# Optimization experiments

Measured on AMD Instinct MI355X. Metric: run time of the kernel, lower is better.

Reference implementation:

```python
import jax, jax.numpy as jnp
from jax import lax
import numpy as np

DIM = 800
FEAT = 192
LAYERS = 5
BLOCK_SZ = [32, 192, 192, 192, 192]
BLOCK_RNG = [0, 32, 224, 416, 608, 800]
HALF = 27  # image_size//4//2 - 1 with image_size=224
EPS = 1e-5


def conv2d(x, w, stride=1, pad=0, groups=1):
    return lax.conv_general_dilated(
        x, w, (stride, stride), [(pad, pad), (pad, pad)],
        dimension_numbers=("NCHW", "OIHW", "NCHW"),
        feature_group_count=groups)


def _bcast(v):
    return v[None, :, None, None]


def setup_inputs() -> dict:
    key = jax.random.key(0)
    ks = jax.random.split(key, 22)
    B = 32
    s = 0.05
    return {
        "x": jax.random.normal(ks[0], (B, 3, 224, 224), jnp.float32),
        "ds_w1": jax.random.normal(ks[1], (16, 3, 3, 3), jnp.float32) * s,
        "ds_b1": jax.random.normal(ks[2], (16,), jnp.float32) * s,
        "bn1_g": jax.random.uniform(ks[3], (16,), jnp.float32) + 0.5,
        "bn1_b": jax.random.normal(ks[4], (16,), jnp.float32) * s,
        "bn1_m": jax.random.normal(ks[5], (16,), jnp.float32) * s,
        "bn1_v": jax.random.uniform(ks[6], (16,), jnp.float32) + 0.5,
        "ds_dw": jax.random.normal(ks[7], (16, 1, 3, 3), jnp.float32) * s,
        "ds_dwb": jax.random.normal(ks[8], (16,), jnp.float32) * s,
        "ds_w2": jax.random.normal(ks[9], (32, 16, 1, 1), jnp.float32) * s,
        "ds_b2": jax.random.normal(ks[10], (32,), jnp.float32) * s,
        "bn2_g": jax.random.uniform(ks[11], (32,), jnp.float32) + 0.5,
        "bn2_b": jax.random.normal(ks[12], (32,), jnp.float32) * s,
        "bn2_m": jax.random.normal(ks[13], (32,), jnp.float32) * s,
        "bn2_v": jax.random.uniform(ks[14], (32,), jnp.float32) + 0.5,
        "conv_dw": jax.random.normal(ks[15], (DIM, 1, 3, 3), jnp.float32) * s,
        "gw": jax.random.normal(ks[16], (DIM, DIM), jnp.float32) * s,
        "in_gamma": jax.random.uniform(ks[17], (DIM,), jnp.float32) + 0.5,
        "in_beta": jax.random.normal(ks[18], (DIM,), jnp.float32) * s,
        "fc_w": jax.random.normal(ks[19], (1000, FEAT), jnp.float32) * s,
        "fc_b": jax.random.normal(ks[20], (1000,), jnp.float32) * s,
    }


def _forward(x, ds_w1, ds_b1, bn1_g, bn1_b, bn1_m, bn1_v, ds_dw, ds_dwb,
             ds_w2, ds_b2, bn2_g, bn2_b, bn2_m, bn2_v, conv_dw, gw,
             in_gamma, in_beta, fc_w, fc_b):
    # ---- downsample stem: conv3x3 s2 -> BN -> ReLU -> dwconv3x3 s2 -> conv1x1 -> BN
    h = conv2d(x, ds_w1, 2, 1) + _bcast(ds_b1)
    h = (h - _bcast(bn1_m)) * _bcast(bn1_g * lax.rsqrt(bn1_v + EPS)) + _bcast(bn1_b)
    h = jax.nn.relu(h)
    h = conv2d(h, ds_dw, 2, 1, groups=16) + _bcast(ds_dwb)
    h = conv2d(h, ds_w2, 1, 0) + _bcast(ds_b2)
    h = (h - _bcast(bn2_m)) * _bcast(bn2_g * lax.rsqrt(bn2_v + EPS)) + _bcast(bn2_b)
    B, _, H, W = h.shape  # (B, 32, 56, 56)
    h = jnp.concatenate([h, jnp.zeros((B, DIM - 32, H, W), h.dtype)], axis=1)

    # ---- per-block InstanceNorm -> ReLU -> depthwise conv -> sliced 1x1 graph conv -> residual
    for i in range(LAYERS):
        s, r0, r1 = BLOCK_SZ[i], BLOCK_RNG[i], BLOCK_RNG[i + 1]
        xa = h[:, :s]
        mu = xa.mean((2, 3), keepdims=True)
        var = ((xa - mu) ** 2).mean((2, 3), keepdims=True)
        xa = (xa - mu) * lax.rsqrt(var + EPS)
        xa = xa * _bcast(in_gamma[r0:r1]) + _bcast(in_beta[r0:r1])
        xa = jax.nn.relu(xa)
        xa = conv2d(xa, conv_dw[r0:r1], 1, 1, groups=s)
        row0 = min(r1, DIM - FEAT)
        xa = jnp.einsum("oc,bchw->bohw", gw[row0:, r0:r1], xa)
        h = (h[:, s:] if i < LAYERS - 1 else h[:, -FEAT:]) + xa

    # ---- AvgPool2d(2) over the 3x3 crop keeps only the top-left 2x2 mean
    out = h[:, :, HALF - 1:HALF + 1, HALF - 1:HALF + 1].mean((2, 3))
    return out @ fc_w.T + fc_b


def reference(x, ds_w1, ds_b1, bn1_g, bn1_b, bn1_m, bn1_v, ds_dw, ds_dwb,
              ds_w2, ds_b2, bn2_g, bn2_b, bn2_m, bn2_v, conv_dw, gw,
              in_gamma, in_beta, fc_w, fc_b):
    return _forward(x, ds_w1, ds_b1, bn1_g, bn1_b, bn1_m, bn1_v, ds_dw, ds_dwb,
                    ds_w2, ds_b2, bn2_g, bn2_b, bn2_m, bn2_v, conv_dw, gw,
                    in_gamma, in_beta, fc_w, fc_b)
```

## Files before the change

### kernel.cpp

```cpp
#include <hip/hip_runtime.h>
#include <stddef.h>

#define EPS 1e-5f
#define N_HW 3136
#define G 32
#define NG (G * N_HW)
#define DIMC 800
#define NTILE 49

typedef unsigned short u16;
typedef __attribute__((ext_vector_type(8))) short short8;
typedef __attribute__((ext_vector_type(4))) float floatx4;

__device__ __forceinline__ u16 f2b(float f) {
  unsigned u = __float_as_uint(f);
  u += 0x7FFFu + ((u >> 16) & 1u);
  return (u16)(u >> 16);
}
__device__ __forceinline__ float blo(unsigned u) { return __uint_as_float(u << 16); }
__device__ __forceinline__ float bhi(unsigned u) { return __uint_as_float(u & 0xFFFF0000u); }

static const size_t XA_OFF  = 0;
static const size_t H0_OFF  = 122028032ull;
static const size_t BLK_OFF = 134873088ull;
static const size_t GWB_OFF = 173408256ull;
static const size_t STS_OFF = 174688256ull;
static const size_t STQ_OFF = 174712832ull;
static const size_t PAT_OFF = 174737408ull;
static const size_t M4_OFF  = 179456000ull;
static const size_t MH_OFF  = M4_OFF + 6144 * 4;
static const size_t OP_OFF  = MH_OFF + 6144 * 4;
static const size_t NEED    = OP_OFF + 6144 * 4;

__global__ __launch_bounds__(256) void gw2bf(const float* __restrict__ gw, u16* __restrict__ gwb) {
  int i = (blockIdx.x * 256 + threadIdx.x) * 4;
  float4 v = *(const float4*)(gw + i);
  gwb[i + 0] = f2b(v.x); gwb[i + 1] = f2b(v.y);
  gwb[i + 2] = f2b(v.z); gwb[i + 3] = f2b(v.w);
}

__global__ __launch_bounds__(256) void zero_stats(float* __restrict__ p) {
  p[blockIdx.x * 256 + threadIdx.x] = 0.f;
}

#define XT_PITCH 226
#define XT_CH (17 * XT_PITCH)
__global__ __launch_bounds__(256) void stem_conv1(
    const float* __restrict__ xg, const float* __restrict__ w, const float* __restrict__ b1,
    const float* __restrict__ g, const float* __restrict__ bb,
    const float* __restrict__ m, const float* __restrict__ v,
    float* __restrict__ h1) {
  __shared__ float xt[3 * XT_CH];
  __shared__ float wt[16 * 27];
  __shared__ float mulc[16], addc[16];
  int blk = blockIdx.x;
  int s = blk % 14;
  int bg = blk / 14;
  int tid = threadIdx.x;

  for (int e = tid; e < 432; e += 256) wt[e] = w[e];
  if (tid < 16) {
    float A = g[tid] * rsqrtf(v[tid] + EPS);
    mulc[tid] = A;
    addc[tid] = (b1[tid] - m[tid]) * A + bb[tid];
  }
  int iy0 = 16 * s - 1;
  for (int e = tid; e < 3 * XT_CH; e += 256) {
    int ci = e / XT_CH;
    int rem = e - ci * XT_CH;
    int r = rem / XT_PITCH;
    int cc = rem - r * XT_PITCH;
    int iy = iy0 + r, ix = cc - 1;
    float val = 0.f;
    if (iy >= 0 && iy < 224 && ix >= 0 && ix < 224)
      val = xg[((size_t)(bg * 3 + ci)) * 224 * 224 + iy * 224 + ix];
    xt[e] = val;
  }
  __syncthreads();

  for (int p = tid; p < 8 * 112; p += 256) {
    int oyl = p / 112, ox = p - oyl * 112;
    float xv[27];
#pragma unroll
    for (int ci = 0; ci < 3; ci++)
#pragma unroll
      for (int ky = 0; ky < 3; ky++)
#pragma unroll
        for (int kx = 0; kx < 3; kx++)
          xv[ci * 9 + ky * 3 + kx] = xt[ci * XT_CH + (2 * oyl + ky) * XT_PITCH + 2 * ox + kx];
    int oy = 8 * s + oyl;
#pragma unroll
    for (int c = 0; c < 16; c++) {
      float acc = 0.f;
#pragma unroll
      for (int t = 0; t < 27; t++) acc += xv[t] * wt[c * 27 + t];
      float y = acc * mulc[c] + addc[c];
      h1[(size_t)(c * G + bg) * 12544 + oy * 112 + ox] = fmaxf(y, 0.f);
    }
  }
}

__global__ __launch_bounds__(256) void stem_dw(
    const float* __restrict__ h1, const float* __restrict__ dw, const float* __restrict__ dwb,
    float* __restrict__ h2) {
  int idx = blockIdx.x * 256 + threadIdx.x;
  int q = idx % N_HW;
  int t = idx / N_HW;
  int bg = t & (G - 1);
  int c = t >> 5;
  int qy = q / 56, qx = q % 56;
  const float* plane = h1 + (size_t)(c * G + bg) * 12544;
  float acc = dwb[c];
#pragma unroll
  for (int ky = 0; ky < 3; ky++) {
    int iy = qy * 2 - 1 + ky;
    if (iy < 0 || iy >= 112) continue;
#pragma unroll
    for (int kx = 0; kx < 3; kx++) {
      int ix = qx * 2 - 1 + kx;
      if (ix < 0 || ix >= 112) continue;
      acc += plane[iy * 112 + ix] * dw[c * 9 + ky * 3 + kx];
    }
  }
  h2[idx] = acc;
}

__global__ __launch_bounds__(256) void stem_pw(
    const float* __restrict__ h2, const float* __restrict__ w2, const float* __restrict__ b2,
    const float* __restrict__ g, const float* __restrict__ bb,
    const float* __restrict__ m, const float* __restrict__ v,
    float* __restrict__ H0) {
  int idx = blockIdx.x * 256 + threadIdx.x;
  int q = idx % N_HW;
  int t = idx / N_HW;
  int bg = t & (G - 1);
  int o = t >> 5;
  float acc = b2[o];
#pragma unroll
  for (int c = 0; c < 16; c++) acc += w2[o * 16 + c] * h2[(size_t)(c * G + bg) * N_HW + q];
  float y = (acc - m[o]) * (g[o] * rsqrtf(v[o] + EPS)) + bb[o];
  H0[idx] = y;
}

template <typename T>
__global__ __launch_bounds__(256) void dw_fused(
    const T* __restrict__ base, const float* __restrict__ cdw,
    const float* __restrict__ in_g, const float* __restrict__ in_b,
    u16* __restrict__ XA, int cdwoff) {
  __shared__ float sm[58 * 58];
  __shared__ float wred[8];
  int blk = blockIdx.x;
  int cl = blk >> 5;
  int c = cdwoff + cl;
  int tid = threadIdx.x;

  if (tid < 58) { sm[tid] = 0.f; sm[57 * 58 + tid] = 0.f; }
  if (tid >= 64 && tid < 120) { int r = tid - 63; sm[r * 58] = 0.f; sm[r * 58 + 57] = 0.f; }

  const T* row = base + (size_t)blk * N_HW;
  float s = 0.f, s2 = 0.f;
  for (int i = tid; i < 392; i += 256) {
    float vals[8];
    if constexpr (sizeof(T) == 2) {
      uint4 u = *(const uint4*)((const u16*)row + i * 8);
      vals[0] = blo(u.x); vals[1] = bhi(u.x);
      vals[2] = blo(u.y); vals[3] = bhi(u.y);
      vals[4] = blo(u.z); vals[5] = bhi(u.z);
      vals[6] = blo(u.w); vals[7] = bhi(u.w);
    } else {
      float4 v0 = *(const float4*)((const float*)row + i * 8);
      float4 v1 = *(const float4*)((const float*)row + i * 8 + 4);
      vals[0] = v0.x; vals[1] = v0.y; vals[2] = v0.z; vals[3] = v0.w;
      vals[4] = v1.x; vals[5] = v1.y; vals[6] = v1.z; vals[7] = v1.w;
    }
    int p = i * 8;
    int y = p / 56, x = p - y * 56;
    float* d = &sm[(y + 1) * 58 + x + 1];
#pragma unroll
    for (int e = 0; e < 8; e++) {
      d[e] = vals[e];
      s += vals[e];
      s2 += vals[e] * vals[e];
    }
  }
#pragma unroll
  for (int o = 32; o > 0; o >>= 1) {
    s += __shfl_down(s, o);
    s2 += __shfl_down(s2, o);
  }
  if ((tid & 63) == 0) { wred[(tid >> 6) * 2] = s; wred[(tid >> 6) * 2 + 1] = s2; }
  __syncthreads();
  float ts = (wred[0] + wred[2]) + (wred[4] + wred[6]);
  float tq = (wred[1] + wred[3]) + (wred[5] + wred[7]);
  float mean = ts * (1.f / N_HW);
  float var = fmaxf(tq * (1.f / N_HW) - mean * mean, 0.f);
  float sc = in_g[c] * rsqrtf(var + EPS);
  float sh = in_b[c] - mean * sc;

  for (int i = tid; i < N_HW; i += 256) {
    int y = i / 56, x = i - y * 56;
    int pos = (y + 1) * 58 + x + 1;
    sm[pos] = fmaxf(sm[pos] * sc + sh, 0.f);
  }
  __syncthreads();

  float w0 = cdw[c * 9 + 0], w1 = cdw[c * 9 + 1], w2 = cdw[c * 9 + 2];
  float w3 = cdw[c * 9 + 3], w4 = cdw[c * 9 + 4], w5 = cdw[c * 9 + 5];
  float w6 = cdw[c * 9 + 6], w7 = cdw[c * 9 + 7], w8 = cdw[c * 9 + 8];
  u16* outp = XA + (size_t)blk * N_HW;
  for (int pp = tid; pp < N_HW / 2; pp += 256) {
    int p = pp * 2;
    int y = p / 56, x = p - y * 56;
    const float* p0 = &sm[y * 58 + x];
    float a0 = p0[0] * w0 + p0[1] * w1 + p0[2] * w2
             + p0[58] * w3 + p0[59] * w4 + p0[60] * w5
             + p0[116] * w6 + p0[117] * w7 + p0[118] * w8;
    float a1 = p0[1] * w0 + p0[2] * w1 + p0[3] * w2
             + p0[59] * w3 + p0[60] * w4 + p0[61] * w5
             + p0[117] * w6 + p0[118] * w7 + p0[119] * w8;
    unsigned pk = (unsigned)f2b(a0) | ((unsigned)f2b(a1) << 16);
    *(unsigned*)&outp[p] = pk;
  }
}

template <int MODE>
__global__ __launch_bounds__(256) void gemm_mfma(
    const u16* __restrict__ A, const u16* __restrict__ B, u16* __restrict__ C,
    float* __restrict__ statS, float* __restrict__ statQ, float* __restrict__ patchf,
    int K) {
  __shared__ u16 As[2][96][40];
  __shared__ u16 Bs[2][32][64];
  int nwg = gridDim.x;
  int cpx = nwg >> 3;
  int j = (blockIdx.x & 7) * cpx + (blockIdx.x >> 3);
  int jm = j & 1;
  int jc = j >> 1;
  int n0 = jc * 64;
  int m0 = jm * 96;
  int tid = threadIdx.x;
  int wave = tid >> 6, lane = tid & 63;
  int wm = wave >> 1, wn = wave & 1;
  int lg = lane >> 4, li = lane & 15;
  floatx4 acc[3][2] = {};

  int ar = tid >> 2, ak = (tid & 3) * 8;
  int bk = tid >> 3, bn = (tid & 7) * 8;
  int bnx = bn ^ ((bk >> 3) << 4);
  const u16* Ag = A + (size_t)(m0 + ar) * DIMC + ak;
  const u16* Bg = B + (size_t)bk * NG + n0 + bn;

  int nt = K / 32;
  uint4 ra0 = *(const uint4*)(Ag);
  uint4 ra1 = {0, 0, 0, 0};
  if (ar < 32) ra1 = *(const uint4*)(Ag + (size_t)64 * DIMC);
  uint4 rb_w = *(const uint4*)(Bg);
  uint4 rb_f = (nt > 1) ? *(const uint4*)(Bg + (size_t)32 * NG) : rb_w;

  for (int t = 0; t < nt; t++) {
    int cur = t & 1;
    *(uint4*)&As[cur][ar][ak] = ra0;
    if (ar < 32) *(uint4*)&As[cur][ar + 64][ak] = ra1;
    *(uint4*)&Bs[cur][bk][bnx] = rb_w;
    uint4 rb_new;
    bool pfA = (t + 1 < nt);
    bool pfB = (t + 2 < nt);
    if (pfA) {
      const u16* ag = Ag + (size_t)(t + 1) * 32;
      ra0 = *(const uint4*)(ag);
      if (ar < 32) ra1 = *(const uint4*)(ag + (size_t)64 * DIMC);
    }
    if (pfB)
      rb_new = *(const uint4*)(Bg + (size_t)(t + 2) * 32 * NG);
    __syncthreads();
    short8 aF[3];
#pragma unroll
    for (int mi = 0; mi < 3; mi++)
      aF[mi] = *(const short8*)&As[cur][wm * 48 + mi * 16 + li][lg * 8];
#pragma unroll
    for (int ni = 0; ni < 2; ni++) {
      int colx = ((wn * 32 + ni * 16) ^ (lg << 4)) + li;
      short8 bF;
#pragma unroll
      for (int e = 0; e < 8; e++) bF[e] = (short)Bs[cur][lg * 8 + e][colx];
#pragma unroll
      for (int mi = 0; mi < 3; mi++)
        acc[mi][ni] = __builtin_amdgcn_mfma_f32_16x16x32_bf16(aF[mi], bF, acc[mi][ni], 0, 0, 0);
    }
    __syncthreads();
    rb_w = rb_f;
    if (pfB) rb_f = rb_new;
  }

  if constexpr (MODE == 0) {
#pragma unroll
    for (int mi = 0; mi < 3; mi++) {
#pragma unroll
      for (int ni = 0; ni < 2; ni++) {
        int row = m0 + wm * 48 + mi * 16 + lg * 4;
        int col = n0 + wn * 32 + ni * 16 + li;
        u16* cp = C + (size_t)row * NG + col;
#pragma unroll
        for (int r = 0; r < 4; r++) cp[(size_t)r * NG] = f2b(acc[mi][ni][r]);
      }
    }
  } else {
    int bg = jc / NTILE;
    int tile = jc % NTILE;
#pragma unroll
    for (int mi = 0; mi < 3; mi++) {
#pragma unroll
      for (int r = 0; r < 4; r++) {
        float v0 = acc[mi][0][r], v1 = acc[mi][1][r];
        float s = v0 + v1;
        float q = v0 * v0 + v1 * v1;
#pragma unroll
        for (int msk = 1; msk < 16; msk <<= 1) {
          s += __shfl_xor(s, msk);
          q += __shfl_xor(q, msk);
        }
        if (li == 0) {
          int row = m0 + wm * 48 + mi * 16 + lg * 4 + r;
          atomicAdd(&statS[row * 32 + bg], s);
          atomicAdd(&statQ[row * 32 + bg], q);
        }
      }
    }
    if (tile >= 22 && tile <= 24) {
#pragma unroll
      for (int mi = 0; mi < 3; mi++) {
#pragma unroll
        for (int ni = 0; ni < 2; ni++) {
          int row = m0 + wm * 48 + mi * 16 + lg * 4;
          int pc = (tile - 22) * 64 + wn * 32 + ni * 16 + li;
#pragma unroll
          for (int r = 0; r < 4; r++)
            patchf[((size_t)(row + r) * 32 + bg) * 192 + pc] = acc[mi][ni][r];
        }
      }
    }
  }
}

__global__ __launch_bounds__(256) void head_m4(
    const float* __restrict__ statS, const float* __restrict__ statQ,
    const float* __restrict__ patchf,
    const float* __restrict__ in_g, const float* __restrict__ in_b,
    const float* __restrict__ cdw, float* __restrict__ m4, float* __restrict__ meanH) {
  int idx = blockIdx.x * 256 + threadIdx.x;
  if (idx >= 192 * 32) return;
  int cl = idx >> 5;
  int c = 608 + cl;
  float mean = statS[idx] * (1.f / N_HW);
  float var = fmaxf(statQ[idx] * (1.f / N_HW) - mean * mean, 0.f);
  float sc = in_g[c] * rsqrtf(var + EPS);
  float sh = in_b[c] - mean * sc;
  const float* pf = patchf + (size_t)idx * 192;
  float val[4][4];
#pragma unroll
  for (int dy = 0; dy < 4; dy++)
#pragma unroll
    for (int dx = 0; dx < 4; dx++) {
      int hw = (25 + dy) * 56 + 25 + dx;
      float v = pf[((hw >> 6) - 22) * 64 + (hw & 63)];
      val[dy][dx] = fmaxf(v * sc + sh, 0.f);
    }
  const float* w = cdw + c * 9;
  float acc = 0.f;
#pragma unroll
  for (int oy = 1; oy < 3; oy++)
#pragma unroll
    for (int ox = 1; ox < 3; ox++)
#pragma unroll
      for (int ky = 0; ky < 3; ky++)
#pragma unroll
        for (int kx = 0; kx < 3; kx++)
          acc += val[oy + ky - 1][ox + kx - 1] * w[ky * 3 + kx];
  m4[idx] = acc * 0.25f;
  float mh = 0.f;
#pragma unroll
  for (int dy = 0; dy < 2; dy++)
#pragma unroll
    for (int dx = 0; dx < 2; dx++) {
      int hw = (26 + dy) * 56 + 26 + dx;
      mh += pf[((hw >> 6) - 22) * 64 + (hw & 63)];
    }
  meanH[idx] = mh * 0.25f;
}

__global__ __launch_bounds__(256) void head_mix(
    const float* __restrict__ gw, const float* __restrict__ m4, const float* __restrict__ meanH,
    float* __restrict__ out_pre) {
  int idx = blockIdx.x * 256 + threadIdx.x;
  if (idx >= G * 192) return;
  int j = idx % 192;
  int bg = idx / 192;
  float acc = meanH[j * G + bg];
  const float* grow = gw + (size_t)(608 + j) * DIMC + 608;
  for (int c = 0; c < 192; c++) acc += grow[c] * m4[c * G + bg];
  out_pre[idx] = acc;
}

__global__ __launch_bounds__(256) void head_fc(
    const float* __restrict__ out_pre, const float* __restrict__ fc_w,
    const float* __restrict__ fc_b, float* __restrict__ outg) {
  int idx = blockIdx.x * 256 + threadIdx.x;
  if (idx >= G * 1000) return;
  int t = idx % 1000;
  int bg = idx / 1000;
  float acc = fc_b[t];
  const float* wr = fc_w + (size_t)t * 192;
  const float* hr = out_pre + (size_t)bg * 192;
  for (int j = 0; j < 192; j++) acc += wr[j] * hr[j];
  outg[idx] = acc;
}

extern "C" void kernel_launch(void* const* d_in, const int* in_sizes, int n_in,
                              void* d_out, int out_size, void* d_ws, size_t ws_size,
                              hipStream_t stream) {
  const float* x      = (const float*)d_in[0];
  const float* ds_w1  = (const float*)d_in[1];
  const float* ds_b1  = (const float*)d_in[2];
  const float* bn1_g  = (const float*)d_in[3];
  const float* bn1_b  = (const float*)d_in[4];
  const float* bn1_m  = (const float*)d_in[5];
  const float* bn1_v  = (const float*)d_in[6];
  const float* ds_dw  = (const float*)d_in[7];
  const float* ds_dwb = (const float*)d_in[8];
  const float* ds_w2  = (const float*)d_in[9];
  const float* ds_b2  = (const float*)d_in[10];
  const float* bn2_g  = (const float*)d_in[11];
  const float* bn2_b  = (const float*)d_in[12];
  const float* bn2_m  = (const float*)d_in[13];
  const float* bn2_v  = (const float*)d_in[14];
  const float* cdw    = (const float*)d_in[15];
  const float* gw     = (const float*)d_in[16];
  const float* in_g   = (const float*)d_in[17];
  const float* in_b   = (const float*)d_in[18];
  const float* fc_w   = (const float*)d_in[19];
  const float* fc_b   = (const float*)d_in[20];
  float* out = (float*)d_out;
  char* ws = (char*)d_ws;

  if (ws_size < NEED) return;

  u16*   XAc    = (u16*)(ws + XA_OFF);
  float* H0     = (float*)(ws + H0_OFF);
  u16*   blockb = (u16*)(ws + BLK_OFF);
  u16*   gwb    = (u16*)(ws + GWB_OFF);
  float* statS  = (float*)(ws + STS_OFF);
  float* statQ  = (float*)(ws + STQ_OFF);
  float* patchf = (float*)(ws + PAT_OFF);
  float* m4     = (float*)(ws + M4_OFF);
  float* meanH  = (float*)(ws + MH_OFF);
  float* opre   = (float*)(ws + OP_OFF);
  float* h1     = (float*)(ws + BLK_OFF);
  float* h2     = h1 + (size_t)16 * G * 12544;

  gw2bf<<<625, 256, 0, stream>>>(gw, gwb);
  zero_stats<<<48, 256, 0, stream>>>(statS);

  static const int CDWOFF[4] = {0, 32, 224, 416};
  static const int SZ[4]     = {32, 192, 192, 192};
  static const int RA[4]     = {32, 224, 416, 608};
  static const int KK[4]     = {32, 224, 416, 608};

  stem_conv1<<<14 * G, 256, 0, stream>>>(
      x, ds_w1, ds_b1, bn1_g, bn1_b, bn1_m, bn1_v, h1);
  stem_dw<<<16 * G * N_HW / 256, 256, 0, stream>>>(h1, ds_dw, ds_dwb, h2);
  stem_pw<<<32 * G * N_HW / 256, 256, 0, stream>>>(
      h2, ds_w2, ds_b2, bn2_g, bn2_b, bn2_m, bn2_v, H0);

  for (int i = 0; i < 4; i++) {
    if (i == 0)
      dw_fused<float><<<SZ[i] * G, 256, 0, stream>>>(
          H0, cdw, in_g, in_b, XAc + (size_t)CDWOFF[i] * NG, CDWOFF[i]);
    else
      dw_fused<u16><<<SZ[i] * G, 256, 0, stream>>>(
          blockb, cdw, in_g, in_b, XAc + (size_t)CDWOFF[i] * NG, CDWOFF[i]);
    if (i < 3)
      gemm_mfma<0><<<NG / 32, 256, 0, stream>>>(
          gwb + (size_t)RA[i] * DIMC, XAc, blockb, nullptr, nullptr, nullptr, KK[i]);
    else
      gemm_mfma<1><<<NG / 32, 256, 0, stream>>>(
          gwb + (size_t)RA[i] * DIMC, XAc, nullptr, statS, statQ, patchf, KK[i]);
  }

  head_m4<<<24, 256, 0, stream>>>(statS, statQ, patchf, in_g, in_b, cdw, m4, meanH);
  head_mix<<<(G * 192 + 255) / 256, 256, 0, stream>>>(gw, m4, meanH, opre);
  head_fc<<<(G * 1000 + 255) / 256, 256, 0, stream>>>(opre, fc_w, fc_b, out);
}
```

Baseline: 393.4 us.

## Process two K-tiles per barrier pair in MFMA GEMM main loop

```diff
diff --git a/kernel.cpp b/kernel.cpp
--- a/kernel.cpp
+++ b/kernel.cpp
@@ -222,6 +222,25 @@
     *(unsigned*)&outp[p] = pk;
   }
 }
+
+#define GEMM_COMPUTE(BUF)                                                       \
+  {                                                                             \
+    short8 aF[3];                                                               \
+    _Pragma("unroll")                                                           \
+    for (int mi = 0; mi < 3; mi++)                                              \
+      aF[mi] = *(const short8*)&As[BUF][wm * 48 + mi * 16 + li][lg * 8];        \
+    _Pragma("unroll")                                                           \
+    for (int ni = 0; ni < 2; ni++) {                                            \
+      int colx = ((wn * 32 + ni * 16) ^ (lg << 4)) + li;                        \
+      short8 bF;                                                                \
+      _Pragma("unroll")                                                         \
+      for (int e = 0; e < 8; e++) bF[e] = (short)Bs[BUF][lg * 8 + e][colx];     \
+      _Pragma("unroll")                                                         \
+      for (int mi = 0; mi < 3; mi++)                                            \
+        acc[mi][ni] = __builtin_amdgcn_mfma_f32_16x16x32_bf16(aF[mi], bF,       \
+                                                              acc[mi][ni], 0, 0, 0); \
+    }                                                                           \
+  }
 
 template <int MODE>
 __global__ __launch_bounds__(256) void gemm_mfma(
@@ -250,45 +269,52 @@
   const u16* Bg = B + (size_t)bk * NG + n0 + bn;
 
   int nt = K / 32;
-  uint4 ra0 = *(const uint4*)(Ag);
-  uint4 ra1 = {0, 0, 0, 0};
-  if (ar < 32) ra1 = *(const uint4*)(Ag + (size_t)64 * DIMC);
-  uint4 rb_w = *(const uint4*)(Bg);
-  uint4 rb_f = (nt > 1) ? *(const uint4*)(Bg + (size_t)32 * NG) : rb_w;
-
-  for (int t = 0; t < nt; t++) {
-    int cur = t & 1;
-    *(uint4*)&As[cur][ar][ak] = ra0;
-    if (ar < 32) *(uint4*)&As[cur][ar + 64][ak] = ra1;
-    *(uint4*)&Bs[cur][bk][bnx] = rb_w;
-    uint4 rb_new;
-    bool pfA = (t + 1 < nt);
-    bool pfB = (t + 2 < nt);
-    if (pfA) {
-      const u16* ag = Ag + (size_t)(t + 1) * 32;
-      ra0 = *(const uint4*)(ag);
-      if (ar < 32) ra1 = *(const uint4*)(ag + (size_t)64 * DIMC);
-    }
-    if (pfB)
-      rb_new = *(const uint4*)(Bg + (size_t)(t + 2) * 32 * NG);
+  bool half = (ar < 32);
+
+  {
+    uint4 p0 = *(const uint4*)(Ag);
+    uint4 p1 = half ? *(const uint4*)(Ag + (size_t)64 * DIMC) : p0;
+    uint4 pb = *(const uint4*)(Bg);
+    *(uint4*)&As[0][ar][ak] = p0;
+    if (half) *(uint4*)&As[0][ar + 64][ak] = p1;
+    *(uint4*)&Bs[0][bk][bnx] = pb;
+  }
+  __syncthreads();
+  uint4 a0A, a1A, bA, a0B, a1B, bB;
+  if (nt > 1) {
+    const u16* ag = Ag + 32;
+    a0A = *(const uint4*)(ag);
+    if (half) a1A = *(const uint4*)(ag + (size_t)64 * DIMC);
+    bA = *(const uint4*)(Bg + (size_t)32 * NG);
+    ag = Ag + 64;
+    a0B = *(const uint4*)(ag);
+    if (half) a1B = *(const uint4*)(ag + (size_t)64 * DIMC);
+    bB = *(const uint4*)(Bg + (size_t)64 * NG);
+  }
+  GEMM_COMPUTE(0);
+  __syncthreads();
+
+  for (int p = 1; p + 1 < nt; p += 2) {
+    *(uint4*)&As[0][ar][ak] = a0A;
+    if (half) *(uint4*)&As[0][ar + 64][ak] = a1A;
+    *(uint4*)&Bs[0][bk][bnx] = bA;
+    *(uint4*)&As[1][ar][ak] = a0B;
+    if (half) *(uint4*)&As[1][ar + 64][ak] = a1B;
+    *(uint4*)&Bs[1][bk][bnx] = bB;
     __syncthreads();
-    short8 aF[3];
-#pragma unroll
-    for (int mi = 0; mi < 3; mi++)
-      aF[mi] = *(const short8*)&As[cur][wm * 48 + mi * 16 + li][lg * 8];
-#pragma unroll
-    for (int ni = 0; ni < 2; ni++) {
-      int colx = ((wn * 32 + ni * 16) ^ (lg << 4)) + li;
-      short8 bF;
-#pragma unroll
-      for (int e = 0; e < 8; e++) bF[e] = (short)Bs[cur][lg * 8 + e][colx];
-#pragma unroll
-      for (int mi = 0; mi < 3; mi++)
-        acc[mi][ni] = __builtin_amdgcn_mfma_f32_16x16x32_bf16(aF[mi], bF, acc[mi][ni], 0, 0, 0);
-    }
+    if (p + 3 < nt) {
+      const u16* ag = Ag + (size_t)(p + 2) * 32;
+      a0A = *(const uint4*)(ag);
+      if (half) a1A = *(const uint4*)(ag + (size_t)64 * DIMC);
+      bA = *(const uint4*)(Bg + (size_t)(p + 2) * 32 * NG);
+      ag = Ag + (size_t)(p + 3) * 32;
+      a0B = *(const uint4*)(ag);
+      if (half) a1B = *(const uint4*)(ag + (size_t)64 * DIMC);
+      bB = *(const uint4*)(Bg + (size_t)(p + 3) * 32 * NG);
+    }
+    GEMM_COMPUTE(0);
+    GEMM_COMPUTE(1);
     __syncthreads();
-    rb_w = rb_f;
-    if (pfB) rb_f = rb_new;
   }
 
   if constexpr (MODE == 0) {
```

Result: faster. 372.3 us (-5.4%).
